# Kernel optimization log

Hardware: AMD Instinct MI355X
Metric: run time of the kernel (lower is better)

The kernel has to match this reference:

```python
import jax, jax.numpy as jnp
import numpy as np

D_MODEL = 1024
N_HEADS = 16
D_HEAD = D_MODEL // N_HEADS
WIN = 256
NEG_INF = -1e30


def setup_inputs() -> dict:
    key = jax.random.key(0)
    k1, k2, k3 = jax.random.split(key, 3)
    B, L = 4, 4096
    x = jax.random.normal(k1, (B, L, D_MODEL), dtype=jnp.float32)
    w_qkv = jax.random.normal(k2, (D_MODEL, 3 * D_MODEL), dtype=jnp.float32) * (1.0 / np.sqrt(D_MODEL))
    w_out = jax.random.normal(k3, (D_MODEL, D_MODEL), dtype=jnp.float32) * (1.0 / np.sqrt(D_MODEL))
    return {"x": x, "w_qkv": w_qkv, "w_out": w_out}


def _band_mask(nb: int):
    ti = jnp.arange(WIN)[:, None]
    tj = jnp.arange(2 * WIN)[None, :]
    base = (tj >= ti + 1) & (tj <= ti + WIN)
    first = base & (tj >= WIN)                         # block 0 has zero-padded (invalid) prev block
    rest = jnp.broadcast_to(base, (nb - 1, WIN, 2 * WIN))
    return jnp.concatenate([first[None], rest], axis=0)


def reference(x, w_qkv, w_out):
    B, L, D = x.shape
    nb = L // WIN
    qkv = (x @ w_qkv).reshape(B, L, 3, N_HEADS, D_HEAD)
    q, k, v = qkv[:, :, 0], qkv[:, :, 1], qkv[:, :, 2]          # [B, L, H, dh]
    def to_blocks(t):
        return t.transpose(0, 2, 1, 3).reshape(B, N_HEADS, nb, WIN, D_HEAD)
    qb, kb, vb = to_blocks(q), to_blocks(k), to_blocks(v)
    zero_blk = jnp.zeros_like(kb[:, :, :1])
    k_kv = jnp.concatenate([jnp.concatenate([zero_blk, kb[:, :, :-1]], axis=2), kb], axis=3)  # [B,H,nb,2W,dh]
    v_kv = jnp.concatenate([jnp.concatenate([zero_blk, vb[:, :, :-1]], axis=2), vb], axis=3)
    scale = 1.0 / np.sqrt(D_HEAD)
    scores = jnp.einsum('bhnqd,bhnkd->bhnqk', qb, k_kv) * scale
    scores = jnp.where(_band_mask(nb), scores, NEG_INF)
    attn = jax.nn.softmax(scores, axis=-1)
    ob = jnp.einsum('bhnqk,bhnkd->bhnqd', attn, v_kv)
    out = ob.reshape(B, N_HEADS, L, D_HEAD).transpose(0, 2, 1, 3).reshape(B, L, D)
    return out @ w_out
```

## Files before the change

kernel.cpp:

```cpp
#include <hip/hip_runtime.h>

typedef __bf16 bf16_t;
typedef __bf16 bf16x8 __attribute__((ext_vector_type(8)));
typedef float f32x4 __attribute__((ext_vector_type(4)));
typedef unsigned short ushort_t;

#define MFMA_16x16x32(a, b, c) __builtin_amdgcn_mfma_f32_16x16x32_bf16((a), (b), (c), 0, 0, 0)

__device__ __forceinline__ void async_ld16(const void* gptr, void* lptr) {
  typedef __attribute__((address_space(1))) const unsigned int as1_t;
  typedef __attribute__((address_space(3))) unsigned int as3_t;
  __builtin_amdgcn_global_load_lds((as1_t*)(unsigned long long)gptr,
                                   (as3_t*)(unsigned int)(unsigned long long)lptr,
                                   16, 0, 0);
}

__global__ void detect_dtype(const ushort_t* __restrict__ x, int* __restrict__ flag) {
  __shared__ int cnt[256];
  int c = 0;
#pragma unroll
  for (int i = 0; i < 16; ++i) {
    const ushort_t u = x[threadIdx.x * 16 + i];
    const int e = (u >> 7) & 0xFF;
    if ((u & 0x7FFF) != 0 && (e < 0x3A || e > 0xC0)) ++c;
  }
  cnt[threadIdx.x] = c;
  __syncthreads();
  if (threadIdx.x == 0) {
    int t = 0;
    for (int i = 0; i < 256; ++i) t += cnt[i];
    *flag = (t > 512) ? 1 : 0;
  }
}

__global__ __launch_bounds__(256) void convert_to_bf16(const void* __restrict__ src,
                                                       bf16_t* __restrict__ dst, int n8,
                                                       const int* __restrict__ flag) {
  const int isF32 = *flag;
  int i = blockIdx.x * 256 + threadIdx.x;
  const int stride = gridDim.x * 256;
  if (isF32) {
    const float4* s = (const float4*)src;
    for (; i < n8; i += stride) {
      const float4 a = s[(size_t)i * 2];
      const float4 b = s[(size_t)i * 2 + 1];
      bf16x8 o;
      o[0] = (bf16_t)a.x; o[1] = (bf16_t)a.y; o[2] = (bf16_t)a.z; o[3] = (bf16_t)a.w;
      o[4] = (bf16_t)b.x; o[5] = (bf16_t)b.y; o[6] = (bf16_t)b.z; o[7] = (bf16_t)b.w;
      *(bf16x8*)(dst + (size_t)i * 8) = o;
    }
  } else {
    const uint4* s = (const uint4*)src;
    for (; i < n8; i += stride) ((uint4*)dst)[i] = s[i];
  }
}

__global__ __launch_bounds__(256) void transpose_b16(const ushort_t* __restrict__ in,
                                                     ushort_t* __restrict__ out,
                                                     int R, int C) {
  __shared__ alignas(16) ushort_t t[64 * 72];
  const int tid = threadIdx.x;
  const int c0 = blockIdx.x * 64;
  const int r0 = blockIdx.y * 64;
#pragma unroll
  for (int it = 0; it < 2; ++it) {
    int cid = tid + it * 256;
    int row = cid >> 3, co = (cid & 7) * 8;
    *(uint4*)(t + row * 72 + co) = *(const uint4*)(in + (size_t)(r0 + row) * C + c0 + co);
  }
  __syncthreads();
#pragma unroll
  for (int it = 0; it < 2; ++it) {
    int cid = tid + it * 256;
    int orow = cid >> 3, ko = (cid & 7) * 8;
    uint4 u;
    ushort_t* tp = (ushort_t*)&u;
#pragma unroll
    for (int j = 0; j < 8; ++j) tp[j] = t[(ko + j) * 72 + orow];
    *(uint4*)(out + (size_t)(c0 + orow) * R + r0 + ko) = u;
  }
}

__global__ __launch_bounds__(256) void transpose_v(const ushort_t* __restrict__ qkv,
                                                   ushort_t* __restrict__ vT) {
  __shared__ alignas(16) ushort_t t[64 * 72];
  const int tid = threadIdx.x;
  const int l0 = blockIdx.x * 64;
  const int bh = blockIdx.y;
  const int b = bh >> 4, h = bh & 15;
  const ushort_t* src = qkv + ((size_t)(b * 4096 + l0)) * 3072 + 2048 + h * 64;
#pragma unroll
  for (int it = 0; it < 2; ++it) {
    int cid = tid + it * 256;
    int row = cid >> 3, co = (cid & 7) * 8;
    *(uint4*)(t + row * 72 + co) = *(const uint4*)(src + (size_t)row * 3072 + co);
  }
  __syncthreads();
  ushort_t* dst = vT + ((size_t)bh * 64) * 4096 + l0;
#pragma unroll
  for (int it = 0; it < 2; ++it) {
    int cid = tid + it * 256;
    int d = cid >> 3, ko = (cid & 7) * 8;
    uint4 u;
    ushort_t* tp = (ushort_t*)&u;
#pragma unroll
    for (int j = 0; j < 8; ++j) tp[j] = t[(ko + j) * 72 + d];
    *(uint4*)(dst + (size_t)d * 4096 + ko) = u;
  }
}

__global__ __launch_bounds__(256) void gemm_bf16(const bf16_t* __restrict__ A, int lda,
                                                 const bf16_t* __restrict__ Bt,
                                                 void* __restrict__ Cout, int N_out,
                                                 int K, const int* __restrict__ flag) {
  __shared__ alignas(16) bf16_t smem[8192];
  bf16_t* a_lds = smem;
  bf16_t* b_lds = smem + 4096;
  const int tid = threadIdx.x;
  const int wave = tid >> 6;
  const int lane = tid & 63;
  const int l15 = lane & 15;
  const int quad = lane >> 4;
  const int tm = blockIdx.y * 128;
  const int tn = blockIdx.x * 128;
  const int wm = (wave >> 1) * 64;
  const int wn = (wave & 1) * 64;

  f32x4 acc[4][4];
#pragma unroll
  for (int i = 0; i < 4; ++i)
#pragma unroll
    for (int j = 0; j < 4; ++j) acc[i][j] = (f32x4){0.f, 0.f, 0.f, 0.f};

  const int srow = wave * 32 + (lane >> 2);
  const int scol = (lane & 3) * 8;
  const bf16_t* ag = A + (size_t)(tm + srow) * lda + scol;
  const bf16_t* bg = Bt + (size_t)(tn + srow) * K + scol;
  bf16_t* al = a_lds + (wave * 32) * 32;
  bf16_t* bl = b_lds + (wave * 32) * 32;

  for (int k0 = 0; k0 < K; k0 += 32) {
    __syncthreads();
    async_ld16(ag, al);
    async_ld16(ag + (size_t)16 * lda, al + 16 * 32);
    async_ld16(bg, bl);
    async_ld16(bg + (size_t)16 * K, bl + 16 * 32);
    ag += 32;
    bg += 32;
    __syncthreads();

    bf16x8 af[4], bfr[4];
#pragma unroll
    for (int i = 0; i < 4; ++i)
      af[i] = *(const bf16x8*)(a_lds + (wm + i * 16 + l15) * 32 + quad * 8);
#pragma unroll
    for (int j = 0; j < 4; ++j)
      bfr[j] = *(const bf16x8*)(b_lds + (wn + j * 16 + l15) * 32 + quad * 8);
#pragma unroll
    for (int i = 0; i < 4; ++i)
#pragma unroll
      for (int j = 0; j < 4; ++j) acc[i][j] = MFMA_16x16x32(af[i], bfr[j], acc[i][j]);
  }
  __syncthreads();

  const int isF32 = flag ? *flag : 0;
  if (isF32) {
#pragma unroll
    for (int i = 0; i < 4; ++i) {
      const int m = tm + wm + i * 16 + quad * 4;
#pragma unroll
      for (int j = 0; j < 4; ++j) {
        const int n = tn + wn + j * 16 + l15;
        float* cp = (float*)Cout + (size_t)m * N_out + n;
#pragma unroll
        for (int r = 0; r < 4; ++r) cp[(size_t)r * N_out] = acc[i][j][r];
      }
    }
  } else {
    bf16_t* stg = smem + wave * 1152;
#pragma unroll
    for (int i = 0; i < 4; ++i) {
#pragma unroll
      for (int j = 0; j < 4; ++j)
#pragma unroll
        for (int r = 0; r < 4; ++r)
          stg[(quad * 4 + r) * 72 + j * 16 + l15] = (bf16_t)acc[i][j][r];
      __asm__ volatile("s_waitcnt lgkmcnt(0)" ::: "memory");
      const int m0 = tm + wm + i * 16;
#pragma unroll
      for (int p = 0; p < 2; ++p) {
        const int idx = lane + p * 64;
        const int row = idx >> 3, c8 = (idx & 7) * 8;
        uint4 u = *(const uint4*)(stg + row * 72 + c8);
        *(uint4*)((bf16_t*)Cout + (size_t)(m0 + row) * N_out + tn + wn + c8) = u;
      }
      __asm__ volatile("s_waitcnt lgkmcnt(0)" ::: "memory");
    }
  }
}

__global__ __launch_bounds__(256) void attn_swa(bf16_t* qkv, const bf16_t* __restrict__ vT) {
  __shared__ alignas(16) bf16_t k_lds[64 * 72];
  __shared__ alignas(16) bf16_t vt_lds[64 * 72];
  __shared__ alignas(16) bf16_t p_lds[4 * 16 * 72];

  const int wg = blockIdx.x;
  const int b = wg >> 10;
  const int h = (wg >> 6) & 15;
  const int qt = wg & 63;
  const int blk = qt >> 2;
  const int wq = qt & 3;
  const int tid = threadIdx.x;
  const int wave = tid >> 6;
  const int lane = tid & 63;
  const int l15 = lane & 15;
  const int quad = lane >> 4;
  const int qw = qt * 64 + wave * 16;

  const size_t qoff = ((size_t)(b * 4096 + qw + l15)) * 3072 + h * 64;
  const bf16x8 qf0 = *(const bf16x8*)(qkv + qoff + quad * 8);
  const bf16x8 qf1 = *(const bf16x8*)(qkv + qoff + 32 + quad * 8);

  f32x4 of[4];
#pragma unroll
  for (int i = 0; i < 4; ++i) of[i] = (f32x4){0.f, 0.f, 0.f, 0.f};
  float m_i[4], l_i[4];
#pragma unroll
  for (int r = 0; r < 4; ++r) {
    m_i[r] = -1e30f;
    l_i[r] = 0.0f;
  }

  const int kb0 = blk * 256 - 256;
  const int kclo = (blk == 0) ? 4 : wq;
  const int kchi = wq + 4;

  for (int kc = kclo; kc <= kchi; ++kc) {
    const int kb = kb0 + kc * 64;
    __syncthreads();
#pragma unroll
    for (int it = 0; it < 2; ++it) {
      int cid = tid + it * 256;
      int row = cid >> 3;
      int co = (cid & 7) * 8;
      *(uint4*)(k_lds + row * 72 + co) =
          *(const uint4*)(qkv + ((size_t)(b * 4096 + kb + row)) * 3072 + 1024 + h * 64 + co);
      *(uint4*)(vt_lds + row * 72 + co) =
          *(const uint4*)(vT + (((size_t)b * 16 + h) * 64 + row) * 4096 + kb + co);
    }
    __syncthreads();

    f32x4 s[4];
#pragma unroll
    for (int nt = 0; nt < 4; ++nt) {
      bf16x8 kf0 = *(const bf16x8*)(k_lds + (nt * 16 + l15) * 72 + quad * 8);
      bf16x8 kf1 = *(const bf16x8*)(k_lds + (nt * 16 + l15) * 72 + 32 + quad * 8);
      f32x4 z = (f32x4){0.f, 0.f, 0.f, 0.f};
      z = MFMA_16x16x32(qf0, kf0, z);
      z = MFMA_16x16x32(qf1, kf1, z);
      s[nt] = z;
    }

    float sv[4][4];
#pragma unroll
    for (int nt = 0; nt < 4; ++nt) {
      const int key = kb + nt * 16 + l15;
#pragma unroll
      for (int r = 0; r < 4; ++r) {
        const int p = qw + quad * 4 + r;
        const bool valid = (key <= p) && (key + 256 > p);
        sv[nt][r] = valid ? s[nt][r] * 0.125f : -1e30f;
      }
    }
    float rm[4];
#pragma unroll
    for (int r = 0; r < 4; ++r)
      rm[r] = fmaxf(fmaxf(sv[0][r], sv[1][r]), fmaxf(sv[2][r], sv[3][r]));
#pragma unroll
    for (int off = 1; off < 16; off <<= 1)
#pragma unroll
      for (int r = 0; r < 4; ++r) rm[r] = fmaxf(rm[r], __shfl_xor(rm[r], off));

    float mn[4], alpha[4];
#pragma unroll
    for (int r = 0; r < 4; ++r) {
      mn[r] = fmaxf(m_i[r], rm[r]);
      alpha[r] = __expf(m_i[r] - mn[r]);
      m_i[r] = mn[r];
    }

    float rs[4] = {0.f, 0.f, 0.f, 0.f};
#pragma unroll
    for (int nt = 0; nt < 4; ++nt)
#pragma unroll
      for (int r = 0; r < 4; ++r) {
        const float pv = (sv[nt][r] > -1e29f) ? __expf(sv[nt][r] - mn[r]) : 0.0f;
        rs[r] += pv;
        p_lds[wave * 1152 + (quad * 4 + r) * 72 + nt * 16 + l15] = (bf16_t)pv;
      }
#pragma unroll
    for (int off = 1; off < 16; off <<= 1)
#pragma unroll
      for (int r = 0; r < 4; ++r) rs[r] += __shfl_xor(rs[r], off);
#pragma unroll
    for (int r = 0; r < 4; ++r) l_i[r] = l_i[r] * alpha[r] + rs[r];
#pragma unroll
    for (int dt = 0; dt < 4; ++dt)
#pragma unroll
      for (int r = 0; r < 4; ++r) of[dt][r] *= alpha[r];

    __syncthreads();

#pragma unroll
    for (int kk = 0; kk < 2; ++kk) {
      bf16x8 pf = *(const bf16x8*)(p_lds + wave * 1152 + l15 * 72 + kk * 32 + quad * 8);
#pragma unroll
      for (int dt = 0; dt < 4; ++dt) {
        bf16x8 vf = *(const bf16x8*)(vt_lds + (dt * 16 + l15) * 72 + kk * 32 + quad * 8);
        of[dt] = MFMA_16x16x32(pf, vf, of[dt]);
      }
    }
  }

  float inv[4];
#pragma unroll
  for (int r = 0; r < 4; ++r) inv[r] = 1.0f / fmaxf(l_i[r], 1e-20f);
  bf16_t* op = qkv + ((size_t)(b * 4096 + qw)) * 3072 + h * 64;
#pragma unroll
  for (int dt = 0; dt < 4; ++dt)
#pragma unroll
    for (int r = 0; r < 4; ++r)
      op[(size_t)(quad * 4 + r) * 3072 + dt * 16 + l15] = (bf16_t)(of[dt][r] * inv[r]);
}

extern "C" void kernel_launch(void* const* d_in, const int* in_sizes, int n_in,
                              void* d_out, int out_size, void* d_ws, size_t ws_size,
                              hipStream_t stream) {
  char* ws = (char*)d_ws;
  bf16_t* wTq = (bf16_t*)(ws);
  bf16_t* wTo = (bf16_t*)(ws + 6291456);
  bf16_t* qkv = (bf16_t*)(ws + 8388608);
  int* flag = (int*)(ws + 109051904);

  bf16_t* xb = (bf16_t*)d_out;
  bf16_t* vTb = (bf16_t*)d_out;
  bf16_t* tmpq = qkv;
  bf16_t* tmpo = qkv + 3145728;

  detect_dtype<<<1, 256, 0, stream>>>((const ushort_t*)d_in[0], flag);
  convert_to_bf16<<<1024, 256, 0, stream>>>(d_in[0], xb, 2097152, flag);
  convert_to_bf16<<<512, 256, 0, stream>>>(d_in[1], tmpq, 393216, flag);
  convert_to_bf16<<<256, 256, 0, stream>>>(d_in[2], tmpo, 131072, flag);
  transpose_b16<<<dim3(48, 16), 256, 0, stream>>>((const ushort_t*)tmpq, (ushort_t*)wTq,
                                                  1024, 3072);
  transpose_b16<<<dim3(16, 16), 256, 0, stream>>>((const ushort_t*)tmpo, (ushort_t*)wTo,
                                                  1024, 1024);
  gemm_bf16<<<dim3(24, 128), 256, 0, stream>>>(xb, 1024, wTq, qkv, 3072, 1024, nullptr);
  transpose_v<<<dim3(64, 64), 256, 0, stream>>>((const ushort_t*)qkv, (ushort_t*)vTb);
  attn_swa<<<dim3(4096), 256, 0, stream>>>(qkv, vTb);
  gemm_bf16<<<dim3(8, 128), 256, 0, stream>>>(qkv, 3072, wTo, d_out, 1024, 1024, flag);
}
```

Measured before the change: 437.5 us.

## Rewrite bf16 GEMM with 256x256 tiles, double-buffered LDS and phased prefetch

Replaces the 128x128 tile GEMM with a 512-thread, 256x256 tile kernel that double-buffers 64-wide K slices in 128KB of LDS. It uses XOR swizzling to avoid bank conflicts, prefetches the next slice in four phases interleaved with MFMA groups using waitcnt, barriers and setprio, and remaps workgroups for L2 locality. The goal is to hide global load latency and raise arithmetic intensity in both projections. In exchange it uses far more LDS and registers, leaves only one workgroup per CU, and produces fewer workgroups for the smaller output GEMM.

```diff
diff --git a/kernel.cpp b/kernel.cpp
--- a/kernel.cpp
+++ b/kernel.cpp
@@ -109,94 +109,179 @@
   }
 }
 
-__global__ __launch_bounds__(256) void gemm_bf16(const bf16_t* __restrict__ A, int lda,
+__global__ __launch_bounds__(512) void gemm_bf16(const bf16_t* __restrict__ A, int lda,
                                                  const bf16_t* __restrict__ Bt,
                                                  void* __restrict__ Cout, int N_out,
                                                  int K, const int* __restrict__ flag) {
-  __shared__ alignas(16) bf16_t smem[8192];
-  bf16_t* a_lds = smem;
-  bf16_t* b_lds = smem + 4096;
+  __shared__ alignas(16) bf16_t smem[65536];
   const int tid = threadIdx.x;
   const int wave = tid >> 6;
   const int lane = tid & 63;
   const int l15 = lane & 15;
   const int quad = lane >> 4;
-  const int tm = blockIdx.y * 128;
-  const int tn = blockIdx.x * 128;
-  const int wm = (wave >> 1) * 64;
-  const int wn = (wave & 1) * 64;
-
-  f32x4 acc[4][4];
-#pragma unroll
-  for (int i = 0; i < 4; ++i)
+  const int wm = wave >> 2;
+  const int wn = wave & 3;
+
+  int lin = blockIdx.y * gridDim.x + blockIdx.x;
+  const int nwg = gridDim.x * gridDim.y;
+  if ((nwg & 7) == 0) lin = (lin & 7) * (nwg >> 3) + (lin >> 3);
+  const int tn = (lin % gridDim.x) * 256;
+  const int tm = (lin / gridDim.x) * 256;
+
+  f32x4 acc[8][4];
+#pragma unroll
+  for (int i = 0; i < 8; ++i)
 #pragma unroll
     for (int j = 0; j < 4; ++j) acc[i][j] = (f32x4){0.f, 0.f, 0.f, 0.f};
 
-  const int srow = wave * 32 + (lane >> 2);
-  const int scol = (lane & 3) * 8;
-  const bf16_t* ag = A + (size_t)(tm + srow) * lda + scol;
-  const bf16_t* bg = Bt + (size_t)(tn + srow) * K + scol;
-  bf16_t* al = a_lds + (wave * 32) * 32;
-  bf16_t* bl = b_lds + (wave * 32) * 32;
-
-  for (int k0 = 0; k0 < K; k0 += 32) {
-    __syncthreads();
-    async_ld16(ag, al);
-    async_ld16(ag + (size_t)16 * lda, al + 16 * 32);
-    async_ld16(bg, bl);
-    async_ld16(bg + (size_t)16 * K, bl + 16 * 32);
-    ag += 32;
-    bg += 32;
-    __syncthreads();
-
-    bf16x8 af[4], bfr[4];
-#pragma unroll
-    for (int i = 0; i < 4; ++i)
-      af[i] = *(const bf16x8*)(a_lds + (wm + i * 16 + l15) * 32 + quad * 8);
-#pragma unroll
-    for (int j = 0; j < 4; ++j)
-      bfr[j] = *(const bf16x8*)(b_lds + (wn + j * 16 + l15) * 32 + quad * 8);
-#pragma unroll
-    for (int i = 0; i < 4; ++i)
-#pragma unroll
-      for (int j = 0; j < 4; ++j) acc[i][j] = MFMA_16x16x32(af[i], bfr[j], acc[i][j]);
-  }
+  const int r_st = tid >> 3;
+  const int jg8 = ((tid & 7) ^ (r_st & 7)) * 8;
+  const int wofs = wave * 512;
+
+  const int rowA = wm * 16 + l15;
+  const int rowB = wn * 16 + l15;
+  const int sw = l15 & 7;
+  const int c0 = (quad ^ sw) * 8;
+  const int c1 = ((quad | 4) ^ sw) * 8;
+
+  const int NT = K >> 6;
+
+#define STAGE_HALF(G, ldg, grow0, kk, ldsbase)                              \
+  do {                                                                      \
+    const bf16_t* _g = (G) + (size_t)((grow0) + r_st) * (ldg) + (kk) + jg8; \
+    async_ld16(_g, &smem[(ldsbase) + wofs]);                                \
+    async_ld16(_g + (size_t)64 * (ldg), &smem[(ldsbase) + 4096 + wofs]);    \
+  } while (0)
+
+#define READ_A(mh)                                                \
+  do {                                                            \
+    _Pragma("unroll") for (int q = 0; q < 4; ++q) {               \
+      const int off = bufA + (((mh)*128 + q * 32 + rowA) << 6);   \
+      a_[q][0] = *(const bf16x8*)&smem[off + c0];                 \
+      a_[q][1] = *(const bf16x8*)&smem[off + c1];                 \
+    }                                                             \
+  } while (0)
+
+#define READ_B(nh)                                                \
+  do {                                                            \
+    _Pragma("unroll") for (int jn = 0; jn < 2; ++jn) {            \
+      const int off = bufB + (((nh)*128 + jn * 64 + rowB) << 6);  \
+      b_[jn][0] = *(const bf16x8*)&smem[off + c0];                \
+      b_[jn][1] = *(const bf16x8*)&smem[off + c1];                \
+    }                                                             \
+  } while (0)
+
+#define DO_MFMA(mh, nh)                                                      \
+  do {                                                                       \
+    _Pragma("unroll") for (int q = 0; q < 4; ++q)                            \
+        _Pragma("unroll") for (int jn = 0; jn < 2; ++jn) {                   \
+      acc[(mh)*4 + q][(nh)*2 + jn] =                                         \
+          MFMA_16x16x32(a_[q][0], b_[jn][0], acc[(mh)*4 + q][(nh)*2 + jn]);  \
+      acc[(mh)*4 + q][(nh)*2 + jn] =                                         \
+          MFMA_16x16x32(a_[q][1], b_[jn][1], acc[(mh)*4 + q][(nh)*2 + jn]);  \
+    }                                                                        \
+  } while (0)
+
+#define PHASE_MID(VMC)                                     \
+  asm volatile("s_waitcnt vmcnt(" VMC ")" ::: "memory");   \
+  __builtin_amdgcn_s_barrier();                            \
+  asm volatile("s_waitcnt lgkmcnt(0)" ::: "memory");       \
+  __builtin_amdgcn_sched_barrier(0);                       \
+  __builtin_amdgcn_s_setprio(1)
+
+#define PHASE_END()               \
+  __builtin_amdgcn_s_setprio(0);  \
+  __builtin_amdgcn_s_barrier();   \
+  __builtin_amdgcn_sched_barrier(0)
+
+  STAGE_HALF(A, lda, tm, 0, 0);
+  STAGE_HALF(Bt, K, tn, 0, 16384);
+  STAGE_HALF(Bt, K, tn + 128, 0, 16384 + 8192);
+  STAGE_HALF(A, lda, tm + 128, 0, 8192);
+  asm volatile("s_waitcnt vmcnt(4)" ::: "memory");
+  __builtin_amdgcn_s_barrier();
+
+  bf16x8 a_[4][2], b_[2][2];
+  int bufA = 0;
+  for (int t = 0; t < NT; ++t) {
+    const int bufB = bufA + 16384;
+    const int sA = bufA ^ 32768;
+    const int sB = sA + 16384;
+    int kst = (t + 1) << 6;
+    if (kst == K) kst = 0;
+
+    READ_A(0);
+    READ_B(0);
+    STAGE_HALF(A, lda, tm, kst, sA);
+    PHASE_MID("4");
+    DO_MFMA(0, 0);
+    PHASE_END();
+
+    READ_B(1);
+    STAGE_HALF(Bt, K, tn, kst, sB);
+    PHASE_MID("4");
+    DO_MFMA(0, 1);
+    PHASE_END();
+
+    READ_A(1);
+    STAGE_HALF(Bt, K, tn + 128, kst, sB + 8192);
+    PHASE_MID("6");
+    DO_MFMA(1, 1);
+    PHASE_END();
+
+    READ_B(0);
+    STAGE_HALF(A, lda, tm + 128, kst, sA + 8192);
+    PHASE_MID("4");
+    DO_MFMA(1, 0);
+    PHASE_END();
+
+    bufA ^= 32768;
+  }
+
+  asm volatile("s_waitcnt vmcnt(0)" ::: "memory");
   __syncthreads();
 
   const int isF32 = flag ? *flag : 0;
   if (isF32) {
 #pragma unroll
-    for (int i = 0; i < 4; ++i) {
-      const int m = tm + wm + i * 16 + quad * 4;
-#pragma unroll
-      for (int j = 0; j < 4; ++j) {
-        const int n = tn + wn + j * 16 + l15;
-        float* cp = (float*)Cout + (size_t)m * N_out + n;
-#pragma unroll
-        for (int r = 0; r < 4; ++r) cp[(size_t)r * N_out] = acc[i][j][r];
+    for (int f = 0; f < 8; ++f) {
+      const int m0 = tm + (f >> 2) * 128 + (f & 3) * 32 + wm * 16 + quad * 4;
+#pragma unroll
+      for (int nidx = 0; nidx < 4; ++nidx) {
+        const int col = tn + (nidx >> 1) * 128 + (nidx & 1) * 64 + wn * 16 + l15;
+        float* cp = (float*)Cout + (size_t)m0 * N_out + col;
+#pragma unroll
+        for (int r = 0; r < 4; ++r) cp[(size_t)r * N_out] = acc[f][nidx][r];
       }
     }
   } else {
     bf16_t* stg = smem + wave * 1152;
 #pragma unroll
-    for (int i = 0; i < 4; ++i) {
-#pragma unroll
-      for (int j = 0; j < 4; ++j)
+    for (int f = 0; f < 8; ++f) {
+#pragma unroll
+      for (int nidx = 0; nidx < 4; ++nidx)
 #pragma unroll
         for (int r = 0; r < 4; ++r)
-          stg[(quad * 4 + r) * 72 + j * 16 + l15] = (bf16_t)acc[i][j][r];
+          stg[(quad * 4 + r) * 72 + nidx * 16 + l15] = (bf16_t)acc[f][nidx][r];
       __asm__ volatile("s_waitcnt lgkmcnt(0)" ::: "memory");
-      const int m0 = tm + wm + i * 16;
+      const int m0 = tm + (f >> 2) * 128 + (f & 3) * 32 + wm * 16;
 #pragma unroll
       for (int p = 0; p < 2; ++p) {
         const int idx = lane + p * 64;
         const int row = idx >> 3, c8 = (idx & 7) * 8;
         uint4 u = *(const uint4*)(stg + row * 72 + c8);
-        *(uint4*)((bf16_t*)Cout + (size_t)(m0 + row) * N_out + tn + wn + c8) = u;
+        const int col = tn + ((c8 >> 5) << 7) + (((c8 >> 4) & 1) << 6) + wn * 16 + (c8 & 15);
+        *(uint4*)((bf16_t*)Cout + (size_t)(m0 + row) * N_out + col) = u;
       }
       __asm__ volatile("s_waitcnt lgkmcnt(0)" ::: "memory");
     }
   }
+#undef STAGE_HALF
+#undef READ_A
+#undef READ_B
+#undef DO_MFMA
+#undef PHASE_MID
+#undef PHASE_END
 }
 
 __global__ __launch_bounds__(256) void attn_swa(bf16_t* qkv, const bf16_t* __restrict__ vT) {
@@ -355,8 +440,8 @@
                                                   1024, 3072);
   transpose_b16<<<dim3(16, 16), 256, 0, stream>>>((const ushort_t*)tmpo, (ushort_t*)wTo,
                                                   1024, 1024);
-  gemm_bf16<<<dim3(24, 128), 256, 0, stream>>>(xb, 1024, wTq, qkv, 3072, 1024, nullptr);
+  gemm_bf16<<<dim3(12, 64), 512, 0, stream>>>(xb, 1024, wTq, qkv, 3072, 1024, nullptr);
   transpose_v<<<dim3(64, 64), 256, 0, stream>>>((const ushort_t*)qkv, (ushort_t*)vTb);
   attn_swa<<<dim3(4096), 256, 0, stream>>>(qkv, vTb);
-  gemm_bf16<<<dim3(8, 128), 256, 0, stream>>>(qkv, 3072, wTo, d_out, 1024, 1024, flag);
-}
+  gemm_bf16<<<dim3(4, 64), 512, 0, stream>>>(qkv, 3072, wTo, d_out, 1024, 1024, flag);
+}
```

Measured after the change: 380.2 us. 13.1% less time.
